# Kernel optimization log

Measured on AMD Instinct MI355X. Metric: run time of the kernel, lower is better.

Reference implementation:

```python
import jax, jax.numpy as jnp
import numpy as np
from jax import lax

C, K, G = 256, 3, 8
CG = C // G          # group channels
P = K * K            # sampling points per group
STRIDE, PAD, DIL = 1, 1, 1
OFFSET_SCALE = 1.0
EPS = 1e-5


def setup_inputs() -> dict:
    key = jax.random.key(0)
    ks = jax.random.split(key, 8)
    N, H, W = 4, 64, 64
    return {
        "x": jax.random.normal(ks[0], (N, C, H, W), jnp.float32),
        "dw_w": jax.random.normal(ks[1], (C, 1, K, K), jnp.float32) * 0.1,
        "dw_b": jax.random.normal(ks[2], (C,), jnp.float32) * 0.01,
        "gn_g": jnp.ones((C,), jnp.float32),
        "gn_b": jnp.zeros((C,), jnp.float32),
        "off_w": jax.random.normal(ks[3], (C, G * P * 2), jnp.float32) * 0.01,
        "off_b": jax.random.normal(ks[4], (G * P * 2,), jnp.float32) * 0.1,
        "mask_w": jax.random.normal(ks[5], (C, G * P), jnp.float32) * 0.02,
        "mask_b": jax.random.normal(ks[6], (G * P,), jnp.float32) * 0.02,
    }


def _dcnv3_core(x_nhwc, offset, mask):
    # x_nhwc (N,H,W,C); offset (N,Ho,Wo,G*P*2); mask (N,Ho,Wo,G*P) already softmaxed
    inp = jnp.pad(x_nhwc, ((0, 0), (PAD, PAD), (PAD, PAD), (0, 0)))
    N, Hp, Wp, _ = inp.shape
    Ho = (Hp - (DIL * (K - 1) + 1)) // STRIDE + 1
    Wo = (Wp - (DIL * (K - 1) + 1)) // STRIDE + 1
    base = (DIL * (K - 1)) // 2 + 0.5
    ref_y = (base + jnp.arange(Ho, dtype=jnp.float32) * STRIDE) / Hp  # (Ho,)
    ref_x = (base + jnp.arange(Wo, dtype=jnp.float32) * STRIDE) / Wp  # (Wo,)
    # dilation grid; flatten order p = iw*K + ih (matches torch meshgrid(x,y) ij)
    kvals = jnp.arange(K, dtype=jnp.float32) * DIL - (DIL * (K - 1)) // 2
    gx = jnp.repeat(kvals, K) / Wp  # (P,)
    gy = jnp.tile(kvals, K) / Hp    # (P,)
    off = offset.reshape(N, Ho, Wo, G, P, 2)
    # normalized sampling locations in [0,1] (then grid_sample convention 2*loc-1)
    loc_x = ref_x[None, None, :, None, None] + gx * OFFSET_SCALE + off[..., 0] * OFFSET_SCALE / Wp
    loc_y = ref_y[None, :, None, None, None] + gy * OFFSET_SCALE + off[..., 1] * OFFSET_SCALE / Hp
    # pixel coords, align_corners=False: px = loc*size - 0.5
    px = loc_x * Wp - 0.5
    py = loc_y * Hp - 0.5
    x0 = jnp.floor(px)
    y0 = jnp.floor(py)
    wx = px - x0
    wy = py - y0
    x0i = x0.astype(jnp.int32)
    y0i = y0.astype(jnp.int32)

    inp_flat = inp.reshape(N, Hp * Wp, G, CG)
    n_idx = jnp.arange(N)[:, None, None, None, None]
    g_idx = jnp.arange(G)[None, None, None, :, None]

    def gather(yi, xi):
        # zeros padding: clamp index, zero out-of-bounds corners
        valid = (yi >= 0) & (yi < Hp) & (xi >= 0) & (xi < Wp)
        idx = jnp.clip(yi, 0, Hp - 1) * Wp + jnp.clip(xi, 0, Wp - 1)
        v = inp_flat[n_idx, idx, g_idx]  # (N,Ho,Wo,G,P,CG)
        return v * valid[..., None]

    m = mask.reshape(N, Ho, Wo, G, P)
    out = jnp.zeros((N, Ho, Wo, G, CG), jnp.float32)
    for dy, dx, w in ((0, 0, (1 - wy) * (1 - wx)), (0, 1, (1 - wy) * wx),
                      (1, 0, wy * (1 - wx)), (1, 1, wy * wx)):
        v = gather(y0i + dy, x0i + dx)
        out = out + jnp.einsum('nhwgp,nhwgpc->nhwgc', m * w, v)
    return out.reshape(N, Ho, Wo, G * CG)


def reference(x, dw_w, dw_b, gn_g, gn_b, off_w, off_b, mask_w, mask_b):
    N, _, H, W = x.shape
    # depthwise 3x3 conv (groups=channels)
    x1 = lax.conv_general_dilated(
        x, dw_w, (1, 1), [((K - 1) // 2, (K - 1) // 2)] * 2,
        dimension_numbers=('NCHW', 'OIHW', 'NCHW'), feature_group_count=C)
    x1 = x1 + dw_b[None, :, None, None]
    # GroupNorm with num_groups=1: normalize over (C,H,W) per sample
    mu = jnp.mean(x1, axis=(1, 2, 3), keepdims=True)
    var = jnp.mean((x1 - mu) ** 2, axis=(1, 2, 3), keepdims=True)
    x1 = (x1 - mu) * lax.rsqrt(var + EPS)
    x1 = x1 * gn_g[None, :, None, None] + gn_b[None, :, None, None]
    x1 = jax.nn.gelu(x1, approximate=False)
    x1 = jnp.transpose(x1, (0, 2, 3, 1))  # NHWC
    offset = x1 @ off_w + off_b                                  # (N,H,W,G*P*2)
    mask = jax.nn.softmax((x1 @ mask_w + mask_b).reshape(N, H, W, G, P), axis=-1)
    mask = mask.reshape(N, H, W, G * P)
    out = _dcnv3_core(jnp.transpose(x, (0, 2, 3, 1)), offset, mask)
    return jnp.transpose(out, (0, 3, 1, 2))  # back to NCHW
```

## Files before the change

### kernel.cpp

```cpp
#include <hip/hip_runtime.h>
#include <math.h>

#define NB   4
#define CH   256
#define HW   4096
#define NCOL 216
#define MTOT 16384
#define CHW  1048576
#define EPSV 1e-5f

#define OFF_NHWC 0
#define NHWCSZ   (NB*HW*CH/2)
#define OFF_OM   (OFF_NHWC + NHWCSZ)
#define OMSZ     (MTOT*NCOL/2)
#define OFF_AB   (OFF_OM + OMSZ)
#define ABSZ     (MTOT*CH/2)
#define OFF_WB   (OFF_AB + ABSZ)
#define WBSZ     (CH*CH/2)
#define OFF_BI   (OFF_WB + WBSZ)
#define OFF_PT   (OFF_BI + 256)

typedef short bf16x8 __attribute__((ext_vector_type(8)));
typedef float f32x4  __attribute__((ext_vector_type(4)));

__device__ __forceinline__ unsigned short f2bf(float f) {
    unsigned int u = __builtin_bit_cast(unsigned int, f);
    u += 0x7fffu + ((u >> 16) & 1u);
    return (unsigned short)(u >> 16);
}

__device__ __forceinline__ float bf2f(unsigned short s) {
    return __builtin_bit_cast(float, (unsigned int)s << 16);
}

__global__ __launch_bounds__(256) void conv_prep_kernel(
    const float* __restrict__ x, const float* __restrict__ dw_w,
    const float* __restrict__ dw_b,
    const float* __restrict__ off_w, const float* __restrict__ off_b,
    const float* __restrict__ mask_w, const float* __restrict__ mask_b,
    unsigned short* __restrict__ A, unsigned short* __restrict__ inp_nhwc,
    unsigned short* __restrict__ Wc_bt, float* __restrict__ bias,
    float* __restrict__ partials) {
    __shared__ float xs[32 * 120];
    __shared__ unsigned short tb[32 * 36];
    __shared__ float rs1[4], rs2[4];
    int b = blockIdx.x;
    int tid = threadIdx.x;
    if (b < 256) {
        int k = b, n = tid;
        float v = 0.f;
        if (n < 144)      v = off_w[k * 144 + n];
        else if (n < 216) v = mask_w[k * 72 + (n - 144)];
        Wc_bt[(size_t)n * 256 + k] = f2bf(v);
        if (b == 0) {
            float bb = 0.f;
            if (n < 144)      bb = off_b[n];
            else if (n < 216) bb = mask_b[n - 144];
            bias[n] = bb;
        }
    }
    int ct  = b & 7;
    int hwt = (b >> 3) & 127;
    int n   = b >> 10;
    int c0 = ct * 32;
    int hw0 = hwt * 32;
    int h  = hw0 >> 6;
    int w0 = hw0 & 63;
    const float* xb = x + ((size_t)n * CH + c0) * HW;
#pragma unroll
    for (int it = 0; it < 3; ++it) {
        int idx = it * 256 + tid;
        int cl  = idx / 24;
        int rem = idx - cl * 24;
        int r   = rem >> 3;
        int f4  = rem & 7;
        int gh  = h - 1 + r;
        float4 v = make_float4(0.f, 0.f, 0.f, 0.f);
        if (gh >= 0 && gh < 64)
            v = *(const float4*)&xb[(size_t)cl * HW + gh * 64 + w0 + f4 * 4];
        *(float4*)&xs[cl * 120 + r * 40 + 4 + f4 * 4] = v;
    }
    if (tid < 192) {
        int cl   = tid / 6;
        int rem  = tid - cl * 6;
        int r    = rem >> 1;
        int side = rem & 1;
        int gh   = h - 1 + r;
        int gw   = side ? (w0 + 32) : (w0 - 1);
        float v = 0.f;
        if (gh >= 0 && gh < 64 && gw >= 0 && gw < 64)
            v = xb[(size_t)cl * HW + gh * 64 + gw];
        xs[cl * 120 + r * 40 + (side ? 36 : 3)] = v;
    }
    __syncthreads();
    int wl = tid & 31;
    int cbase = (tid >> 5) * 4;
    float s1 = 0.f, s2 = 0.f;
    ushort4 o;
    unsigned short ov[4];
#pragma unroll
    for (int j = 0; j < 4; ++j) {
        int c = c0 + cbase + j;
        float acc = dw_b[c];
        const float* wk = dw_w + c * 9;
#pragma unroll
        for (int r = 0; r < 3; ++r)
#pragma unroll
            for (int kx = 0; kx < 3; ++kx)
                acc = fmaf(xs[(cbase + j) * 120 + r * 40 + wl + kx + 3], wk[r * 3 + kx], acc);
        s1 += acc; s2 += acc * acc;
        ov[j] = f2bf(acc);
    }
    o.x = ov[0]; o.y = ov[1]; o.z = ov[2]; o.w = ov[3];
    *(ushort4*)&tb[wl * 36 + cbase] = o;
#pragma unroll
    for (int off = 32; off >= 1; off >>= 1) {
        s1 += __shfl_xor(s1, off, 64);
        s2 += __shfl_xor(s2, off, 64);
    }
    if ((tid & 63) == 0) { rs1[tid >> 6] = s1; rs2[tid >> 6] = s2; }
    {
        int r2 = tid >> 3, cg = tid & 7;
        ushort4 rv;
        rv.x = f2bf(xs[(cg * 4 + 0) * 120 + 40 + r2 + 4]);
        rv.y = f2bf(xs[(cg * 4 + 1) * 120 + 40 + r2 + 4]);
        rv.z = f2bf(xs[(cg * 4 + 2) * 120 + 40 + r2 + 4]);
        rv.w = f2bf(xs[(cg * 4 + 3) * 120 + 40 + r2 + 4]);
        *(ushort4*)&inp_nhwc[((size_t)(n * HW + hw0 + r2)) * 256 + c0 + cg * 4] = rv;
    }
    __syncthreads();
    if (tid == 0) {
        partials[2 * b]     = rs1[0] + rs1[1] + rs1[2] + rs1[3];
        partials[2 * b + 1] = rs2[0] + rs2[1] + rs2[2] + rs2[3];
    }
    int r2 = tid >> 3, cg = tid & 7;
    ushort4 w4 = *(const ushort4*)&tb[r2 * 36 + cg * 4];
    *(ushort4*)&A[((size_t)(n * HW + hw0 + r2)) * 256 + c0 + cg * 4] = w4;
}

#define LDK 72
__global__ __launch_bounds__(512) void fused_gemm_dcn_kernel(
    const unsigned short* __restrict__ A, const unsigned short* __restrict__ Bt,
    const float* __restrict__ bias, const float* __restrict__ partials,
    const float* __restrict__ gn_g, const float* __restrict__ gn_b,
    const unsigned short* __restrict__ inp_nhwc, float* __restrict__ out) {
    __shared__ unsigned short As[64 * LDK];
    __shared__ unsigned short Bs[256 * LDK];
    __shared__ float lom[64 * 216];
    __shared__ float ot[2 * 16 * 260];
    __shared__ float red1[8], red2[8];

    int bid = blockIdx.x;
    int tile = (bid & 7) * 32 + (bid >> 3);
    int m0 = tile * 64;
    int n = m0 >> 12;
    int hwb = m0 & 4095;
    int tid = threadIdx.x, lane = tid & 63, wid = tid >> 6;

#pragma unroll
    for (int i = 0; i < 4; ++i) {
        int q = i * 512 + tid;
        int mm = q >> 3, kk = (q & 7) * 8;
        *(uint4*)&Bs[mm * LDK + kk] = *(const uint4*)&Bt[(size_t)mm * 256 + kk];
    }

    {
        const float2* p2 = (const float2*)partials;
        float2 a = p2[n * 1024 + tid];
        float2 c = p2[n * 1024 + tid + 512];
        float s1 = a.x + c.x, s2 = a.y + c.y;
#pragma unroll
        for (int off = 32; off >= 1; off >>= 1) {
            s1 += __shfl_xor(s1, off, 64);
            s2 += __shfl_xor(s2, off, 64);
        }
        if (lane == 0) { red1[wid] = s1; red2[wid] = s2; }
    }
    __syncthreads();
    float t1 = 0.f, t2 = 0.f;
#pragma unroll
    for (int i = 0; i < 8; ++i) { t1 += red1[i]; t2 += red2[i]; }
    float mean = t1 * (1.f / (float)CHW);
    float var  = t2 * (1.f / (float)CHW) - mean * mean;
    float rsig = rsqrtf(var + EPSV);

    f32x4 acc[4][2] = {};
    for (int k0 = 0; k0 < 256; k0 += 64) {
        {
            int row = tid >> 3, kk0 = (tid & 7) * 8;
            union { uint4 u; unsigned short s[8]; } in, ou;
            in.u = *(const uint4*)&A[((size_t)(m0 + row)) * 256 + k0 + kk0];
#pragma unroll
            for (int j = 0; j < 8; ++j) {
                int ch = k0 + kk0 + j;
                float v = bf2f(in.s[j]);
                v = (v - mean) * rsig * gn_g[ch] + gn_b[ch];
                v = 0.5f * v * (1.0f + erff(v * 0.70710678118654752f));
                ou.s[j] = f2bf(v);
            }
            *(uint4*)&As[row * LDK + kk0] = ou.u;
        }
        if (k0) {
#pragma unroll
            for (int i = 0; i < 4; ++i) {
                int q = i * 512 + tid;
                int mm = q >> 3, kk = (q & 7) * 8;
                *(uint4*)&Bs[mm * LDK + kk] = *(const uint4*)&Bt[(size_t)mm * 256 + k0 + kk];
            }
        }
        __syncthreads();
#pragma unroll
        for (int kh = 0; kh < 2; ++kh) {
            bf16x8 af[4], bfr[2];
#pragma unroll
            for (int mi = 0; mi < 4; ++mi)
                af[mi] = *(const bf16x8*)&As[(mi * 16 + (lane & 15)) * LDK + kh * 32 + (lane >> 4) * 8];
#pragma unroll
            for (int nj = 0; nj < 2; ++nj)
                bfr[nj] = *(const bf16x8*)&Bs[(wid * 32 + nj * 16 + (lane & 15)) * LDK + kh * 32 + (lane >> 4) * 8];
#pragma unroll
            for (int mi = 0; mi < 4; ++mi)
#pragma unroll
                for (int nj = 0; nj < 2; ++nj)
                    acc[mi][nj] = __builtin_amdgcn_mfma_f32_16x16x32_bf16(
                        af[mi], bfr[nj], acc[mi][nj], 0, 0, 0);
        }
        __syncthreads();
    }
#pragma unroll
    for (int nj = 0; nj < 2; ++nj) {
        int col = wid * 32 + nj * 16 + (lane & 15);
        if (col < NCOL) {
            float bcol = bias[col];
#pragma unroll
            for (int mi = 0; mi < 4; ++mi)
#pragma unroll
                for (int r = 0; r < 4; ++r) {
                    int row = mi * 16 + (lane >> 4) * 4 + r;
                    lom[row * NCOL + col] = acc[mi][nj][r] + bcol;
                }
        }
    }
    __syncthreads();

    const unsigned short* base = inp_nhwc + (size_t)n * HW * 256;
    int h = hwb >> 6;
    int half = tid >> 5;
    int l  = tid & 31;
    int g  = l >> 2;
    int ch0 = l * 8;
#pragma unroll
    for (int round = 0; round < 4; ++round) {
        float* otb = &ot[(round & 1) * 16 * 260];
        int pixloc = round * 16 + half;
        int w = pixloc;
        const float* lm = &lom[pixloc * NCOL];
        float lg[9];
        float mx = -1e30f;
#pragma unroll
        for (int p = 0; p < 9; ++p) { lg[p] = lm[144 + g * 9 + p]; mx = fmaxf(mx, lg[p]); }
        float sum = 0.f;
#pragma unroll
        for (int p = 0; p < 9; ++p) { lg[p] = __expf(lg[p] - mx); sum += lg[p]; }
        float rs = 1.0f / sum;
        float acc2[8] = {};
#pragma unroll
        for (int p = 0; p < 9; ++p) {
            float ox = lm[g * 18 + p * 2];
            float oy = lm[g * 18 + p * 2 + 1];
            float px = (float)(w + (p / 3)) + ox;
            float py = (float)(h + (p % 3)) + oy;
            float xf = floorf(px), yf = floorf(py);
            float wx = px - xf, wy = py - yf;
            int x0 = (int)xf, y0 = (int)yf;
            float m = lg[p] * rs;
            float w00 = m * (1.f - wy) * (1.f - wx);
            float w01 = m * (1.f - wy) * wx;
            float w10 = m * wy * (1.f - wx);
            float w11 = m * wy * wx;
#pragma unroll
            for (int corner = 0; corner < 4; ++corner) {
                int yi = y0 + (corner >> 1);
                int xi = x0 + (corner & 1);
                float cw = (corner == 0) ? w00 : (corner == 1) ? w01 : (corner == 2) ? w10 : w11;
                bool valid = (yi >= 1) & (yi <= 64) & (xi >= 1) & (xi <= 64);
                int yc = min(max(yi, 1), 64) - 1;
                int xc = min(max(xi, 1), 64) - 1;
                bf16x8 v = *(const bf16x8*)&base[((size_t)yc * 64 + xc) * 256 + ch0];
                float f = valid ? cw : 0.f;
#pragma unroll
                for (int j = 0; j < 8; ++j)
                    acc2[j] = fmaf(f, bf2f((unsigned short)v[j]), acc2[j]);
            }
        }
        *(float4*)&otb[half * 260 + ch0]     = make_float4(acc2[0], acc2[1], acc2[2], acc2[3]);
        *(float4*)&otb[half * 260 + ch0 + 4] = make_float4(acc2[4], acc2[5], acc2[6], acc2[7]);
        __syncthreads();
        int px = tid & 15, crow = tid >> 4;
#pragma unroll
        for (int cc = 0; cc < 8; ++cc) {
            int c = cc * 32 + crow;
            out[((size_t)(n * CH + c)) * HW + hwb + round * 16 + px] = otb[px * 260 + c];
        }
    }
}

extern "C" void kernel_launch(void* const* d_in, const int* in_sizes, int n_in,
                              void* d_out, int out_size, void* d_ws, size_t ws_size,
                              hipStream_t stream) {
    const float* x      = (const float*)d_in[0];
    const float* dw_w   = (const float*)d_in[1];
    const float* dw_b   = (const float*)d_in[2];
    const float* gn_g   = (const float*)d_in[3];
    const float* gn_b   = (const float*)d_in[4];
    const float* off_w  = (const float*)d_in[5];
    const float* off_b  = (const float*)d_in[6];
    const float* mask_w = (const float*)d_in[7];
    const float* mask_b = (const float*)d_in[8];
    float* out = (float*)d_out;

    float* ws = (float*)d_ws;
    unsigned short* inp_nhwc = (unsigned short*)(ws + OFF_NHWC);
    unsigned short* Abf   = (unsigned short*)(ws + OFF_AB);
    unsigned short* Wc_bt = (unsigned short*)(ws + OFF_WB);
    float* bias     = ws + OFF_BI;
    float* partials = ws + OFF_PT;

    conv_prep_kernel<<<4096, 256, 0, stream>>>(x, dw_w, dw_b, off_w, off_b,
                                               mask_w, mask_b, Abf, inp_nhwc,
                                               Wc_bt, bias, partials);
    fused_gemm_dcn_kernel<<<256, 512, 0, stream>>>(Abf, Wc_bt, bias, partials,
                                                   gn_g, gn_b, inp_nhwc, out);
}
```

Before: 128.3 us.

## Halve fused GEMM+DCN tile to 32 rows, alias shared memory, double block count

The fused GEMM/deformable-sampling kernel now handles 32 output pixels per block instead of 64, and launches 512 blocks instead of 256. Shared memory is packed into one buffer where the output staging area reuses the A/B GEMM tiles, shrinking the per-block footprint. The goal is to fill more CUs and raise occupancy (launch bounds ask for 4 blocks). In exchange, each block reloads the full 256x256 weight matrix for half as much work, and an extra barrier is added between the two output rounds.

```diff
diff --git a/kernel.cpp b/kernel.cpp
--- a/kernel.cpp
+++ b/kernel.cpp
@@ -139,20 +139,28 @@
 }
 
 #define LDK 72
-__global__ __launch_bounds__(512) void fused_gemm_dcn_kernel(
+#define SM_LOM   0
+#define SM_AS    27648
+#define SM_BS    (27648 + 4608)
+#define SM_OT    27648
+#define SM_RED   69120
+#define SM_SZ    69184
+__global__ __launch_bounds__(512, 4) void fused_gemm_dcn_kernel(
     const unsigned short* __restrict__ A, const unsigned short* __restrict__ Bt,
     const float* __restrict__ bias, const float* __restrict__ partials,
     const float* __restrict__ gn_g, const float* __restrict__ gn_b,
     const unsigned short* __restrict__ inp_nhwc, float* __restrict__ out) {
-    __shared__ unsigned short As[64 * LDK];
-    __shared__ unsigned short Bs[256 * LDK];
-    __shared__ float lom[64 * 216];
-    __shared__ float ot[2 * 16 * 260];
-    __shared__ float red1[8], red2[8];
+    __shared__ __align__(16) char smem[SM_SZ];
+    float* lom          = (float*)(smem + SM_LOM);
+    unsigned short* As  = (unsigned short*)(smem + SM_AS);
+    unsigned short* Bs  = (unsigned short*)(smem + SM_BS);
+    float* ot           = (float*)(smem + SM_OT);
+    float* red1         = (float*)(smem + SM_RED);
+    float* red2         = red1 + 8;
 
     int bid = blockIdx.x;
-    int tile = (bid & 7) * 32 + (bid >> 3);
-    int m0 = tile * 64;
+    int tile = (bid & 7) * 64 + (bid >> 3);
+    int m0 = tile * 32;
     int n = m0 >> 12;
     int hwb = m0 & 4095;
     int tid = threadIdx.x, lane = tid & 63, wid = tid >> 6;
@@ -184,21 +192,21 @@
     float var  = t2 * (1.f / (float)CHW) - mean * mean;
     float rsig = rsqrtf(var + EPSV);
 
-    f32x4 acc[4][2] = {};
+    f32x4 acc[2][2] = {};
     for (int k0 = 0; k0 < 256; k0 += 64) {
         {
-            int row = tid >> 3, kk0 = (tid & 7) * 8;
-            union { uint4 u; unsigned short s[8]; } in, ou;
-            in.u = *(const uint4*)&A[((size_t)(m0 + row)) * 256 + k0 + kk0];
-#pragma unroll
-            for (int j = 0; j < 8; ++j) {
+            int row = tid >> 4, kk0 = (tid & 15) * 4;
+            union { uint2 u; unsigned short s[4]; } in, ou;
+            in.u = *(const uint2*)&A[((size_t)(m0 + row)) * 256 + k0 + kk0];
+#pragma unroll
+            for (int j = 0; j < 4; ++j) {
                 int ch = k0 + kk0 + j;
                 float v = bf2f(in.s[j]);
                 v = (v - mean) * rsig * gn_g[ch] + gn_b[ch];
                 v = 0.5f * v * (1.0f + erff(v * 0.70710678118654752f));
                 ou.s[j] = f2bf(v);
             }
-            *(uint4*)&As[row * LDK + kk0] = ou.u;
+            *(uint2*)&As[row * LDK + kk0] = ou.u;
         }
         if (k0) {
 #pragma unroll
@@ -211,15 +219,15 @@
         __syncthreads();
 #pragma unroll
         for (int kh = 0; kh < 2; ++kh) {
-            bf16x8 af[4], bfr[2];
-#pragma unroll
-            for (int mi = 0; mi < 4; ++mi)
+            bf16x8 af[2], bfr[2];
+#pragma unroll
+            for (int mi = 0; mi < 2; ++mi)
                 af[mi] = *(const bf16x8*)&As[(mi * 16 + (lane & 15)) * LDK + kh * 32 + (lane >> 4) * 8];
 #pragma unroll
             for (int nj = 0; nj < 2; ++nj)
                 bfr[nj] = *(const bf16x8*)&Bs[(wid * 32 + nj * 16 + (lane & 15)) * LDK + kh * 32 + (lane >> 4) * 8];
 #pragma unroll
-            for (int mi = 0; mi < 4; ++mi)
+            for (int mi = 0; mi < 2; ++mi)
 #pragma unroll
                 for (int nj = 0; nj < 2; ++nj)
                     acc[mi][nj] = __builtin_amdgcn_mfma_f32_16x16x32_bf16(
@@ -233,7 +241,7 @@
         if (col < NCOL) {
             float bcol = bias[col];
 #pragma unroll
-            for (int mi = 0; mi < 4; ++mi)
+            for (int mi = 0; mi < 2; ++mi)
 #pragma unroll
                 for (int r = 0; r < 4; ++r) {
                     int row = mi * 16 + (lane >> 4) * 4 + r;
@@ -244,16 +252,15 @@
     __syncthreads();
 
     const unsigned short* base = inp_nhwc + (size_t)n * HW * 256;
-    int h = hwb >> 6;
     int half = tid >> 5;
     int l  = tid & 31;
     int g  = l >> 2;
     int ch0 = l * 8;
 #pragma unroll
-    for (int round = 0; round < 4; ++round) {
-        float* otb = &ot[(round & 1) * 16 * 260];
+    for (int round = 0; round < 2; ++round) {
         int pixloc = round * 16 + half;
-        int w = pixloc;
+        int hw = hwb + pixloc;
+        int h = hw >> 6, w = hw & 63;
         const float* lm = &lom[pixloc * NCOL];
         float lg[9];
         float mx = -1e30f;
@@ -293,15 +300,16 @@
                     acc2[j] = fmaf(f, bf2f((unsigned short)v[j]), acc2[j]);
             }
         }
-        *(float4*)&otb[half * 260 + ch0]     = make_float4(acc2[0], acc2[1], acc2[2], acc2[3]);
-        *(float4*)&otb[half * 260 + ch0 + 4] = make_float4(acc2[4], acc2[5], acc2[6], acc2[7]);
+        *(float4*)&ot[half * 260 + ch0]     = make_float4(acc2[0], acc2[1], acc2[2], acc2[3]);
+        *(float4*)&ot[half * 260 + ch0 + 4] = make_float4(acc2[4], acc2[5], acc2[6], acc2[7]);
         __syncthreads();
         int px = tid & 15, crow = tid >> 4;
 #pragma unroll
         for (int cc = 0; cc < 8; ++cc) {
             int c = cc * 32 + crow;
-            out[((size_t)(n * CH + c)) * HW + hwb + round * 16 + px] = otb[px * 260 + c];
-        }
+            out[((size_t)(n * CH + c)) * HW + hwb + round * 16 + px] = ot[px * 260 + c];
+        }
+        if (round == 0) __syncthreads();
     }
 }
 
@@ -329,6 +337,6 @@
     conv_prep_kernel<<<4096, 256, 0, stream>>>(x, dw_w, dw_b, off_w, off_b,
                                                mask_w, mask_b, Abf, inp_nhwc,
                                                Wc_bt, bias, partials);
-    fused_gemm_dcn_kernel<<<256, 512, 0, stream>>>(Abf, Wc_bt, bias, partials,
+    fused_gemm_dcn_kernel<<<512, 512, 0, stream>>>(Abf, Wc_bt, bias, partials,
                                                    gn_g, gn_b, inp_nhwc, out);
 }
```

After: 130.4 us. About the same (+1.7%).
